# Kernel optimization log

Measured on AMD Instinct MI355X. Metric: run time of the kernel, lower is better.

Reference implementation:

```python
import jax, jax.numpy as jnp
import numpy as np
from jax import lax

B, T, D_IN = 512, 256, 64
N_NEURONS, D_STATE, D_OUT = 2048, 64, 10


def setup_inputs() -> dict:
    key = jax.random.key(0)
    k_seq, k_enc, k_bias, k_gain, k_sd, k_d = jax.random.split(key, 6)
    enc = jax.random.normal(k_enc, (N_NEURONS, D_IN + D_STATE), dtype=jnp.float32)
    # hypersphere strategy: unit-norm encoder rows
    enc = enc / jnp.linalg.norm(enc, axis=-1, keepdims=True)
    return {
        "seq": jax.random.normal(k_seq, (B, T, D_IN), dtype=jnp.float32),
        "encoders": enc,
        "bias": jax.random.normal(k_bias, (N_NEURONS,), dtype=jnp.float32),
        "gain": jax.random.uniform(k_gain, (N_NEURONS,), dtype=jnp.float32),
        "state_decoders": jax.random.normal(k_sd, (N_NEURONS, D_STATE), dtype=jnp.float32) * 0.02,
        "decoders": jax.random.normal(k_d, (N_NEURONS, D_OUT), dtype=jnp.float32) * 0.02,
    }


def reference(seq, encoders, bias, gain, state_decoders, decoders):
    # seq: (B, T, d_in). Recurrent decode-then-re-encode loop over T.
    b = seq.shape[0]
    d_state = state_decoders.shape[1]
    n = encoders.shape[0]

    def step(carry, u_t):
        s, _ = carry  # s: (B, d_state)
        x_aug = jnp.concatenate([u_t, s], axis=-1)  # (B, d_in + d_state)
        a = jnp.abs(gain * (x_aug @ encoders.T) + bias)  # (B, n_neurons), activation='abs'
        s_new = a @ state_decoders  # (B, d_state)
        return (s_new, a), None

    s0 = jnp.zeros((b, d_state), dtype=seq.dtype)
    a0 = jnp.zeros((b, n), dtype=seq.dtype)
    (_, a_final), _ = lax.scan(step, (s0, a0), jnp.swapaxes(seq, 0, 1))
    return a_final @ decoders  # (B, d_out)
```

## Files before the change

### kernel.cpp

```cpp
#include <hip/hip_runtime.h>
#include <math.h>

#define B_    512
#define T_    256
#define DIN   64
#define DS    64
#define KK    128
#define NN    2048
#define DOUT  10

#define NT      512
#define BT      8
#define NTILES  (NN / NT)
#define BTILES  (B_ / BT)
#define THREADS 512
#define NWG     (NTILES * BTILES)

#define PSQ_ELEMS  ((size_t)BTILES * NTILES * BT * DS)
#define PS_FLOATS  (4 * PSQ_ELEMS)
#define ETSW_OFF   PS_FLOATS
#define ETSW_F16   ((size_t)KK * NN)
#define SDSW_OFF   (ETSW_OFF + ETSW_F16 / 2)
#define SDSW_F16   ((size_t)NN * DS)

typedef _Float16 half8 __attribute__((ext_vector_type(8)));
typedef float    f32x4 __attribute__((ext_vector_type(4)));

__global__ __launch_bounds__(256) void pre_kernel(const float* __restrict__ enc,
                                                  const float* __restrict__ sd,
                                                  float* __restrict__ ws,
                                                  float* __restrict__ out) {
    size_t i = (size_t)blockIdx.x * blockDim.x + threadIdx.x;
    size_t stride = (size_t)gridDim.x * blockDim.x;
    unsigned long long* psq = (unsigned long long*)ws;
    for (size_t x = i; x < 2 * PSQ_ELEMS; x += stride) psq[x] = 0ull;
    _Float16* EtSw = (_Float16*)(ws + ETSW_OFF);
    for (size_t x = i; x < (size_t)KK * NN; x += stride) {
        const int j     = (int)(x & 7);
        const int lane  = (int)((x >> 3) & 63);
        const int ktile = (int)((x >> 9) & 3);
        const int ntile = (int)((x >> 11) & 3);
        const int w     = (int)((x >> 13) & 7);
        const int nt    = (int)(x >> 16);
        const int n = nt * 512 + w * 64 + ntile * 16 + (lane & 15);
        const int k = ktile * 32 + ((lane >> 4) << 3) + j;
        EtSw[x] = (_Float16)enc[(size_t)n * KK + k];
    }
    _Float16* SdSw = (_Float16*)(ws + SDSW_OFF);
    for (size_t x = i; x < (size_t)NN * DS; x += stride) {
        const int j     = (int)(x & 7);
        const int lane  = (int)((x >> 3) & 63);
        const int ktile = (int)((x >> 9) & 15);
        const int cg    = (int)((x >> 13) & 3);
        const int nt    = (int)(x >> 15);
        const int n = nt * 512 + ktile * 32 + ((lane >> 4) << 3) + j;
        const int c = cg * 16 + (lane & 15);
        SdSw[x] = (_Float16)sd[(size_t)n * DS + c];
    }
    for (size_t x = i; x < (size_t)B_ * DOUT; x += stride) out[x] = 0.0f;
}

__global__ __launch_bounds__(THREADS, 1) void persist_kernel(
    const float* __restrict__ seq,
    const _Float16* __restrict__ EtSw,
    const _Float16* __restrict__ SdSw,
    const float* __restrict__ bias,
    const float* __restrict__ gain,
    const float* __restrict__ dec,
    unsigned long long* __restrict__ psq,
    float* __restrict__ out)
{
    __shared__ _Float16 xh[16][136];
    __shared__ _Float16 Ash[16][520];

    const int tid = threadIdx.x;
    const int nt = blockIdx.x & (NTILES - 1);
    const int bt = blockIdx.x >> 2;
    const int n0 = nt * NT;
    const int b0 = bt * BT;

    const int w = tid >> 6;
    const int l = tid & 63;
    const int rs = tid >> 6;
    const int cs = tid & 63;
    const int m16 = l & 15;
    const int q8  = (l >> 4) << 3;

    const _Float16* EtW = EtSw + ((size_t)(nt * 8 + w) << 13);
    const _Float16* SdW = SdSw + ((size_t)(nt * 4 + (w & 3)) << 13);

    half8 etf[4][4];
    #pragma unroll
    for (int n4 = 0; n4 < 4; ++n4)
        #pragma unroll
        for (int kt = 0; kt < 4; ++kt)
            etf[n4][kt] = *(const half8*)&EtW[(n4 << 11) + (kt << 9) + (size_t)l * 8];
    half8 sdf[16];
    #pragma unroll
    for (int kt = 0; kt < 16; ++kt)
        sdf[kt] = *(const half8*)&SdW[(kt << 9) + (size_t)l * 8];

    float gv[4], bv[4];
    #pragma unroll
    for (int n4 = 0; n4 < 4; ++n4) {
        gv[n4] = gain[n0 + w * 64 + n4 * 16 + m16];
        bv[n4] = bias[n0 + w * 64 + n4 * 16 + m16];
    }

    const size_t fan_base = ((size_t)bt * NTILES) * BT * DS + (size_t)rs * DS + cs;

    {
        unsigned int* xz = (unsigned int*)&xh[0][0];
        for (int i2 = tid; i2 < 16 * 136 / 2; i2 += THREADS) xz[i2] = 0u;
    }
    __syncthreads();
    if (tid < 128) {
        const int r = tid >> 4, c = (tid & 15) << 2;
        const float4 uv = *(const float4*)&seq[((size_t)(b0 + r) * T_ + 0) * DIN + c];
        _Float16* p = &xh[r][c];
        p[0] = (_Float16)uv.x; p[1] = (_Float16)uv.y;
        p[2] = (_Float16)uv.z; p[3] = (_Float16)uv.w;
    }
    __syncthreads();

    for (int t = 0; t < T_; ++t) {
        const unsigned long long* pb =
            psq + (size_t)((t - 1) & 1) * PSQ_ELEMS + fan_base;
        unsigned long long v0 = 0, v1 = 0, v2 = 0, v3 = 0;
        if (t > 0) {
            v0 = __hip_atomic_load(pb + 0 * (BT * DS), __ATOMIC_RELAXED, __HIP_MEMORY_SCOPE_AGENT);
            v1 = __hip_atomic_load(pb + 1 * (BT * DS), __ATOMIC_RELAXED, __HIP_MEMORY_SCOPE_AGENT);
            v2 = __hip_atomic_load(pb + 2 * (BT * DS), __ATOMIC_RELAXED, __HIP_MEMORY_SCOPE_AGENT);
            v3 = __hip_atomic_load(pb + 3 * (BT * DS), __ATOMIC_RELAXED, __HIP_MEMORY_SCOPE_AGENT);
        }

        f32x4 acc[4];
        #pragma unroll
        for (int n4 = 0; n4 < 4; ++n4) acc[n4] = (f32x4){0.f, 0.f, 0.f, 0.f};
        {
            const half8 af0 = *(const half8*)&xh[m16][q8];
            const half8 af1 = *(const half8*)&xh[m16][32 + q8];
            #pragma unroll
            for (int n4 = 0; n4 < 4; ++n4) {
                acc[n4] = __builtin_amdgcn_mfma_f32_16x16x32_f16(af0, etf[n4][0], acc[n4], 0, 0, 0);
                acc[n4] = __builtin_amdgcn_mfma_f32_16x16x32_f16(af1, etf[n4][1], acc[n4], 0, 0, 0);
            }
        }

        if (t > 0) {
            const unsigned utag = (unsigned)t;
            for (;;) {
                if ((unsigned)(v0 >> 32) == utag && (unsigned)(v1 >> 32) == utag &&
                    (unsigned)(v2 >> 32) == utag && (unsigned)(v3 >> 32) == utag)
                    break;
                v0 = __hip_atomic_load(pb + 0 * (BT * DS), __ATOMIC_RELAXED, __HIP_MEMORY_SCOPE_AGENT);
                v1 = __hip_atomic_load(pb + 1 * (BT * DS), __ATOMIC_RELAXED, __HIP_MEMORY_SCOPE_AGENT);
                v2 = __hip_atomic_load(pb + 2 * (BT * DS), __ATOMIC_RELAXED, __HIP_MEMORY_SCOPE_AGENT);
                v3 = __hip_atomic_load(pb + 3 * (BT * DS), __ATOMIC_RELAXED, __HIP_MEMORY_SCOPE_AGENT);
            }
            const float ssum = __uint_as_float((unsigned)v0) + __uint_as_float((unsigned)v1)
                             + __uint_as_float((unsigned)v2) + __uint_as_float((unsigned)v3);
            xh[rs][DIN + cs] = (_Float16)ssum;
        } else {
            xh[rs][DIN + cs] = (_Float16)0.f;
        }
        __syncthreads();

        {
            const half8 af2 = *(const half8*)&xh[m16][64 + q8];
            const half8 af3 = *(const half8*)&xh[m16][96 + q8];
            #pragma unroll
            for (int n4 = 0; n4 < 4; ++n4) {
                acc[n4] = __builtin_amdgcn_mfma_f32_16x16x32_f16(af2, etf[n4][2], acc[n4], 0, 0, 0);
                acc[n4] = __builtin_amdgcn_mfma_f32_16x16x32_f16(af3, etf[n4][3], acc[n4], 0, 0, 0);
            }
        }

        if (l < 32) {
            const int rq = (l >> 4) << 2;
            #pragma unroll
            for (int n4 = 0; n4 < 4; ++n4) {
                const int n = w * 64 + n4 * 16 + m16;
                Ash[rq + 0][n] = (_Float16)fabsf(gv[n4] * acc[n4][0] + bv[n4]);
                Ash[rq + 1][n] = (_Float16)fabsf(gv[n4] * acc[n4][1] + bv[n4]);
                Ash[rq + 2][n] = (_Float16)fabsf(gv[n4] * acc[n4][2] + bv[n4]);
                Ash[rq + 3][n] = (_Float16)fabsf(gv[n4] * acc[n4][3] + bv[n4]);
            }
        }
        __syncthreads();

        if (t == T_ - 1) {
            for (int idx = tid; idx < BT * DOUT; idx += THREADS) {
                const int r = idx / DOUT;
                const int d = idx % DOUT;
                float o = 0.f;
                #pragma unroll 8
                for (int n = 0; n < NT; ++n)
                    o += (float)Ash[r][n] * dec[(size_t)(n0 + n) * DOUT + d];
                atomicAdd(&out[(size_t)(b0 + r) * DOUT + d], o);
            }
            return;
        }

        if (w < 4) {
            f32x4 d0 = (f32x4){0.f, 0.f, 0.f, 0.f};
            f32x4 d1 = (f32x4){0.f, 0.f, 0.f, 0.f};
            #pragma unroll
            for (int kt = 0; kt < 16; kt += 2) {
                const half8 a0 = *(const half8*)&Ash[m16][kt * 32 + q8];
                d0 = __builtin_amdgcn_mfma_f32_16x16x32_f16(a0, sdf[kt], d0, 0, 0, 0);
                const half8 a1 = *(const half8*)&Ash[m16][(kt + 1) * 32 + q8];
                d1 = __builtin_amdgcn_mfma_f32_16x16x32_f16(a1, sdf[kt + 1], d1, 0, 0, 0);
            }
            d0[0] += d1[0]; d0[1] += d1[1]; d0[2] += d1[2]; d0[3] += d1[3];
            if (l < 32) {
                const int rq = (l >> 4) << 2;
                unsigned long long* pw = psq + (size_t)(t & 1) * PSQ_ELEMS
                    + (((size_t)bt * NTILES + nt) * BT) * DS + 16 * w + m16;
                const unsigned long long tg = (unsigned long long)(unsigned)(t + 1) << 32;
                #pragma unroll
                for (int r = 0; r < 4; ++r) {
                    const float v = d0[rq >= 4 ? r : r] + 0.f;
                    const float vv = d0[r];
                    (void)v;
                    __hip_atomic_store(pw + (size_t)(rq + r) * DS,
                                       tg | (unsigned long long)__float_as_uint(vv),
                                       __ATOMIC_RELAXED, __HIP_MEMORY_SCOPE_AGENT);
                }
            }
        } else if (l < 32) {
            const int idx = ((w - 4) << 5) + l;
            const int r = idx >> 4, c = (idx & 15) << 2;
            const float4 uv =
                *(const float4*)&seq[((size_t)(b0 + r) * T_ + (t + 1)) * DIN + c];
            _Float16* p = &xh[r][c];
            p[0] = (_Float16)uv.x; p[1] = (_Float16)uv.y;
            p[2] = (_Float16)uv.z; p[3] = (_Float16)uv.w;
        }
        __syncthreads();
    }
}

extern "C" void kernel_launch(void* const* d_in, const int* in_sizes, int n_in,
                              void* d_out, int out_size, void* d_ws, size_t ws_size,
                              hipStream_t stream) {
    const float* seq  = (const float*)d_in[0];
    const float* enc  = (const float*)d_in[1];
    const float* bias = (const float*)d_in[2];
    const float* gain = (const float*)d_in[3];
    const float* sd   = (const float*)d_in[4];
    const float* dec  = (const float*)d_in[5];
    float* out = (float*)d_out;
    float* ws  = (float*)d_ws;

    pre_kernel<<<dim3(1024), dim3(256), 0, stream>>>(enc, sd, ws, out);

    unsigned long long* psq = (unsigned long long*)ws;
    const _Float16* EtSw = (const _Float16*)(ws + ETSW_OFF);
    const _Float16* SdSw = (const _Float16*)(ws + SDSW_OFF);

    persist_kernel<<<dim3(NWG), dim3(THREADS), 0, stream>>>(
        seq, EtSw, SdSw, bias, gain, dec, psq, out);
}
```

Baseline: 609.0 us.

## Interleave two independent batch chunks per workgroup to hide cross-workgroup sync latency

Each persistent workgroup now owns two 8-row batch chunks and alternates between them within each timestep. While waiting on the state fan-in flags of one chunk, it computes the other chunk, and it prefetches the other chunk's partial-state loads early. This halves the grid, so each workgroup does twice the serial work, in exchange for overlapping the inter-workgroup spin-wait latency with useful MFMA work. It also doubles LDS use and adds barriers per step.

```diff
diff --git a/kernel.cpp b/kernel.cpp
--- a/kernel.cpp
+++ b/kernel.cpp
@@ -12,11 +12,12 @@
 #define NT      512
 #define BT      8
 #define NTILES  (NN / NT)
-#define BTILES  (B_ / BT)
+#define BTE     (B_ / BT)
+#define BTILES  (BTE / 2)
 #define THREADS 512
 #define NWG     (NTILES * BTILES)
 
-#define PSQ_ELEMS  ((size_t)BTILES * NTILES * BT * DS)
+#define PSQ_ELEMS  ((size_t)BTE * NTILES * BT * DS)
 #define PS_FLOATS  (4 * PSQ_ELEMS)
 #define ETSW_OFF   PS_FLOATS
 #define ETSW_F16   ((size_t)KK * NN)
@@ -70,14 +71,19 @@
     unsigned long long* __restrict__ psq,
     float* __restrict__ out)
 {
-    __shared__ _Float16 xh[16][136];
-    __shared__ _Float16 Ash[16][520];
+    __shared__ _Float16 xhA[16][136];
+    __shared__ _Float16 xhB[16][136];
+    __shared__ _Float16 AshA[16][520];
+    __shared__ _Float16 AshB[16][520];
 
     const int tid = threadIdx.x;
     const int nt = blockIdx.x & (NTILES - 1);
     const int bt = blockIdx.x >> 2;
     const int n0 = nt * NT;
-    const int b0 = bt * BT;
+    const int beA = bt * 2;
+    const int beB = bt * 2 + 1;
+    const int b0A = bt * 16;
+    const int b0B = bt * 16 + 8;
 
     const int w = tid >> 6;
     const int l = tid & 63;
@@ -107,87 +113,95 @@
         bv[n4] = bias[n0 + w * 64 + n4 * 16 + m16];
     }
 
-    const size_t fan_base = ((size_t)bt * NTILES) * BT * DS + (size_t)rs * DS + cs;
+    const size_t fanA = ((size_t)beA * NTILES) * BT * DS + (size_t)rs * DS + cs;
+    const size_t fanB = ((size_t)beB * NTILES) * BT * DS + (size_t)rs * DS + cs;
 
     {
-        unsigned int* xz = (unsigned int*)&xh[0][0];
+        unsigned int* xz = (unsigned int*)&xhA[0][0];
         for (int i2 = tid; i2 < 16 * 136 / 2; i2 += THREADS) xz[i2] = 0u;
+        unsigned int* xz2 = (unsigned int*)&xhB[0][0];
+        for (int i2 = tid; i2 < 16 * 136 / 2; i2 += THREADS) xz2[i2] = 0u;
     }
     __syncthreads();
-    if (tid < 128) {
-        const int r = tid >> 4, c = (tid & 15) << 2;
-        const float4 uv = *(const float4*)&seq[((size_t)(b0 + r) * T_ + 0) * DIN + c];
-        _Float16* p = &xh[r][c];
+    if (tid < 256) {
+        const int ch  = tid >> 7;
+        const int idx = tid & 127;
+        const int r = idx >> 4, c = (idx & 15) << 2;
+        const float4 uv =
+            *(const float4*)&seq[((size_t)((ch ? b0B : b0A) + r) * T_ + 0) * DIN + c];
+        _Float16* p = ch ? &xhB[r][c] : &xhA[r][c];
         p[0] = (_Float16)uv.x; p[1] = (_Float16)uv.y;
         p[2] = (_Float16)uv.z; p[3] = (_Float16)uv.w;
     }
     __syncthreads();
 
+    unsigned long long vA0 = 0, vA1 = 0, vA2 = 0, vA3 = 0;
+    unsigned long long vB0 = 0, vB1 = 0, vB2 = 0, vB3 = 0;
+
     for (int t = 0; t < T_; ++t) {
-        const unsigned long long* pb =
-            psq + (size_t)((t - 1) & 1) * PSQ_ELEMS + fan_base;
-        unsigned long long v0 = 0, v1 = 0, v2 = 0, v3 = 0;
-        if (t > 0) {
-            v0 = __hip_atomic_load(pb + 0 * (BT * DS), __ATOMIC_RELAXED, __HIP_MEMORY_SCOPE_AGENT);
-            v1 = __hip_atomic_load(pb + 1 * (BT * DS), __ATOMIC_RELAXED, __HIP_MEMORY_SCOPE_AGENT);
-            v2 = __hip_atomic_load(pb + 2 * (BT * DS), __ATOMIC_RELAXED, __HIP_MEMORY_SCOPE_AGENT);
-            v3 = __hip_atomic_load(pb + 3 * (BT * DS), __ATOMIC_RELAXED, __HIP_MEMORY_SCOPE_AGENT);
-        }
-
         f32x4 acc[4];
         #pragma unroll
         for (int n4 = 0; n4 < 4; ++n4) acc[n4] = (f32x4){0.f, 0.f, 0.f, 0.f};
         {
-            const half8 af0 = *(const half8*)&xh[m16][q8];
-            const half8 af1 = *(const half8*)&xh[m16][32 + q8];
+            const half8 af0 = *(const half8*)&xhA[m16][q8];
+            const half8 af1 = *(const half8*)&xhA[m16][32 + q8];
             #pragma unroll
             for (int n4 = 0; n4 < 4; ++n4) {
                 acc[n4] = __builtin_amdgcn_mfma_f32_16x16x32_f16(af0, etf[n4][0], acc[n4], 0, 0, 0);
                 acc[n4] = __builtin_amdgcn_mfma_f32_16x16x32_f16(af1, etf[n4][1], acc[n4], 0, 0, 0);
             }
         }
-
         if (t > 0) {
+            const unsigned long long* pbA =
+                psq + (size_t)((t - 1) & 1) * PSQ_ELEMS + fanA;
             const unsigned utag = (unsigned)t;
             for (;;) {
-                if ((unsigned)(v0 >> 32) == utag && (unsigned)(v1 >> 32) == utag &&
-                    (unsigned)(v2 >> 32) == utag && (unsigned)(v3 >> 32) == utag)
+                if ((unsigned)(vA0 >> 32) == utag && (unsigned)(vA1 >> 32) == utag &&
+                    (unsigned)(vA2 >> 32) == utag && (unsigned)(vA3 >> 32) == utag)
                     break;
-                v0 = __hip_atomic_load(pb + 0 * (BT * DS), __ATOMIC_RELAXED, __HIP_MEMORY_SCOPE_AGENT);
-                v1 = __hip_atomic_load(pb + 1 * (BT * DS), __ATOMIC_RELAXED, __HIP_MEMORY_SCOPE_AGENT);
-                v2 = __hip_atomic_load(pb + 2 * (BT * DS), __ATOMIC_RELAXED, __HIP_MEMORY_SCOPE_AGENT);
-                v3 = __hip_atomic_load(pb + 3 * (BT * DS), __ATOMIC_RELAXED, __HIP_MEMORY_SCOPE_AGENT);
-            }
-            const float ssum = __uint_as_float((unsigned)v0) + __uint_as_float((unsigned)v1)
-                             + __uint_as_float((unsigned)v2) + __uint_as_float((unsigned)v3);
-            xh[rs][DIN + cs] = (_Float16)ssum;
+                vA0 = __hip_atomic_load(pbA + 0 * (BT * DS), __ATOMIC_RELAXED, __HIP_MEMORY_SCOPE_AGENT);
+                vA1 = __hip_atomic_load(pbA + 1 * (BT * DS), __ATOMIC_RELAXED, __HIP_MEMORY_SCOPE_AGENT);
+                vA2 = __hip_atomic_load(pbA + 2 * (BT * DS), __ATOMIC_RELAXED, __HIP_MEMORY_SCOPE_AGENT);
+                vA3 = __hip_atomic_load(pbA + 3 * (BT * DS), __ATOMIC_RELAXED, __HIP_MEMORY_SCOPE_AGENT);
+            }
+            const float ssum = __uint_as_float((unsigned)vA0) + __uint_as_float((unsigned)vA1)
+                             + __uint_as_float((unsigned)vA2) + __uint_as_float((unsigned)vA3);
+            xhA[rs][DIN + cs] = (_Float16)ssum;
         } else {
-            xh[rs][DIN + cs] = (_Float16)0.f;
+            xhA[rs][DIN + cs] = (_Float16)0.f;
         }
         __syncthreads();
 
         {
-            const half8 af2 = *(const half8*)&xh[m16][64 + q8];
-            const half8 af3 = *(const half8*)&xh[m16][96 + q8];
+            const half8 af2 = *(const half8*)&xhA[m16][64 + q8];
+            const half8 af3 = *(const half8*)&xhA[m16][96 + q8];
             #pragma unroll
             for (int n4 = 0; n4 < 4; ++n4) {
                 acc[n4] = __builtin_amdgcn_mfma_f32_16x16x32_f16(af2, etf[n4][2], acc[n4], 0, 0, 0);
                 acc[n4] = __builtin_amdgcn_mfma_f32_16x16x32_f16(af3, etf[n4][3], acc[n4], 0, 0, 0);
             }
         }
-
         if (l < 32) {
             const int rq = (l >> 4) << 2;
             #pragma unroll
             for (int n4 = 0; n4 < 4; ++n4) {
                 const int n = w * 64 + n4 * 16 + m16;
-                Ash[rq + 0][n] = (_Float16)fabsf(gv[n4] * acc[n4][0] + bv[n4]);
-                Ash[rq + 1][n] = (_Float16)fabsf(gv[n4] * acc[n4][1] + bv[n4]);
-                Ash[rq + 2][n] = (_Float16)fabsf(gv[n4] * acc[n4][2] + bv[n4]);
-                Ash[rq + 3][n] = (_Float16)fabsf(gv[n4] * acc[n4][3] + bv[n4]);
-            }
-        }
-        __syncthreads();
+                AshA[rq + 0][n] = (_Float16)fabsf(gv[n4] * acc[n4][0] + bv[n4]);
+                AshA[rq + 1][n] = (_Float16)fabsf(gv[n4] * acc[n4][1] + bv[n4]);
+                AshA[rq + 2][n] = (_Float16)fabsf(gv[n4] * acc[n4][2] + bv[n4]);
+                AshA[rq + 3][n] = (_Float16)fabsf(gv[n4] * acc[n4][3] + bv[n4]);
+            }
+        }
+        __syncthreads();
+
+        if (t > 0) {
+            const unsigned long long* pbB =
+                psq + (size_t)((t - 1) & 1) * PSQ_ELEMS + fanB;
+            vB0 = __hip_atomic_load(pbB + 0 * (BT * DS), __ATOMIC_RELAXED, __HIP_MEMORY_SCOPE_AGENT);
+            vB1 = __hip_atomic_load(pbB + 1 * (BT * DS), __ATOMIC_RELAXED, __HIP_MEMORY_SCOPE_AGENT);
+            vB2 = __hip_atomic_load(pbB + 2 * (BT * DS), __ATOMIC_RELAXED, __HIP_MEMORY_SCOPE_AGENT);
+            vB3 = __hip_atomic_load(pbB + 3 * (BT * DS), __ATOMIC_RELAXED, __HIP_MEMORY_SCOPE_AGENT);
+        }
 
         if (t == T_ - 1) {
             for (int idx = tid; idx < BT * DOUT; idx += THREADS) {
@@ -196,46 +210,149 @@
                 float o = 0.f;
                 #pragma unroll 8
                 for (int n = 0; n < NT; ++n)
-                    o += (float)Ash[r][n] * dec[(size_t)(n0 + n) * DOUT + d];
-                atomicAdd(&out[(size_t)(b0 + r) * DOUT + d], o);
-            }
-            return;
-        }
-
-        if (w < 4) {
-            f32x4 d0 = (f32x4){0.f, 0.f, 0.f, 0.f};
-            f32x4 d1 = (f32x4){0.f, 0.f, 0.f, 0.f};
-            #pragma unroll
-            for (int kt = 0; kt < 16; kt += 2) {
-                const half8 a0 = *(const half8*)&Ash[m16][kt * 32 + q8];
-                d0 = __builtin_amdgcn_mfma_f32_16x16x32_f16(a0, sdf[kt], d0, 0, 0, 0);
-                const half8 a1 = *(const half8*)&Ash[m16][(kt + 1) * 32 + q8];
-                d1 = __builtin_amdgcn_mfma_f32_16x16x32_f16(a1, sdf[kt + 1], d1, 0, 0, 0);
-            }
-            d0[0] += d1[0]; d0[1] += d1[1]; d0[2] += d1[2]; d0[3] += d1[3];
-            if (l < 32) {
-                const int rq = (l >> 4) << 2;
-                unsigned long long* pw = psq + (size_t)(t & 1) * PSQ_ELEMS
-                    + (((size_t)bt * NTILES + nt) * BT) * DS + 16 * w + m16;
-                const unsigned long long tg = (unsigned long long)(unsigned)(t + 1) << 32;
+                    o += (float)AshA[r][n] * dec[(size_t)(n0 + n) * DOUT + d];
+                atomicAdd(&out[(size_t)(b0A + r) * DOUT + d], o);
+            }
+        } else {
+            if (w < 4) {
+                f32x4 d0 = (f32x4){0.f, 0.f, 0.f, 0.f};
+                f32x4 d1 = (f32x4){0.f, 0.f, 0.f, 0.f};
                 #pragma unroll
-                for (int r = 0; r < 4; ++r) {
-                    const float v = d0[rq >= 4 ? r : r] + 0.f;
-                    const float vv = d0[r];
-                    (void)v;
-                    __hip_atomic_store(pw + (size_t)(rq + r) * DS,
-                                       tg | (unsigned long long)__float_as_uint(vv),
-                                       __ATOMIC_RELAXED, __HIP_MEMORY_SCOPE_AGENT);
+                for (int kt = 0; kt < 16; kt += 2) {
+                    const half8 a0 = *(const half8*)&AshA[m16][kt * 32 + q8];
+                    d0 = __builtin_amdgcn_mfma_f32_16x16x32_f16(a0, sdf[kt], d0, 0, 0, 0);
+                    const half8 a1 = *(const half8*)&AshA[m16][(kt + 1) * 32 + q8];
+                    d1 = __builtin_amdgcn_mfma_f32_16x16x32_f16(a1, sdf[kt + 1], d1, 0, 0, 0);
                 }
-            }
-        } else if (l < 32) {
-            const int idx = ((w - 4) << 5) + l;
-            const int r = idx >> 4, c = (idx & 15) << 2;
-            const float4 uv =
-                *(const float4*)&seq[((size_t)(b0 + r) * T_ + (t + 1)) * DIN + c];
-            _Float16* p = &xh[r][c];
-            p[0] = (_Float16)uv.x; p[1] = (_Float16)uv.y;
-            p[2] = (_Float16)uv.z; p[3] = (_Float16)uv.w;
+                d0[0] += d1[0]; d0[1] += d1[1]; d0[2] += d1[2]; d0[3] += d1[3];
+                if (l < 32) {
+                    const int rq = (l >> 4) << 2;
+                    unsigned long long* pw = psq + (size_t)(t & 1) * PSQ_ELEMS
+                        + (((size_t)beA * NTILES + nt) * BT) * DS + 16 * w + m16;
+                    const unsigned long long tg = (unsigned long long)(unsigned)(t + 1) << 32;
+                    #pragma unroll
+                    for (int r = 0; r < 4; ++r) {
+                        __hip_atomic_store(pw + (size_t)(rq + r) * DS,
+                                           tg | (unsigned long long)__float_as_uint(d0[r]),
+                                           __ATOMIC_RELAXED, __HIP_MEMORY_SCOPE_AGENT);
+                    }
+                }
+            } else if (l < 32) {
+                const int idx = ((w - 4) << 5) + l;
+                const int r = idx >> 4, c = (idx & 15) << 2;
+                const float4 uv =
+                    *(const float4*)&seq[((size_t)(b0A + r) * T_ + (t + 1)) * DIN + c];
+                _Float16* p = &xhA[r][c];
+                p[0] = (_Float16)uv.x; p[1] = (_Float16)uv.y;
+                p[2] = (_Float16)uv.z; p[3] = (_Float16)uv.w;
+            }
+        }
+        __syncthreads();
+
+        #pragma unroll
+        for (int n4 = 0; n4 < 4; ++n4) acc[n4] = (f32x4){0.f, 0.f, 0.f, 0.f};
+        {
+            const half8 af0 = *(const half8*)&xhB[m16][q8];
+            const half8 af1 = *(const half8*)&xhB[m16][32 + q8];
+            #pragma unroll
+            for (int n4 = 0; n4 < 4; ++n4) {
+                acc[n4] = __builtin_amdgcn_mfma_f32_16x16x32_f16(af0, etf[n4][0], acc[n4], 0, 0, 0);
+                acc[n4] = __builtin_amdgcn_mfma_f32_16x16x32_f16(af1, etf[n4][1], acc[n4], 0, 0, 0);
+            }
+        }
+        if (t > 0) {
+            const unsigned long long* pbB =
+                psq + (size_t)((t - 1) & 1) * PSQ_ELEMS + fanB;
+            const unsigned utag = (unsigned)t;
+            for (;;) {
+                if ((unsigned)(vB0 >> 32) == utag && (unsigned)(vB1 >> 32) == utag &&
+                    (unsigned)(vB2 >> 32) == utag && (unsigned)(vB3 >> 32) == utag)
+                    break;
+                vB0 = __hip_atomic_load(pbB + 0 * (BT * DS), __ATOMIC_RELAXED, __HIP_MEMORY_SCOPE_AGENT);
+                vB1 = __hip_atomic_load(pbB + 1 * (BT * DS), __ATOMIC_RELAXED, __HIP_MEMORY_SCOPE_AGENT);
+                vB2 = __hip_atomic_load(pbB + 2 * (BT * DS), __ATOMIC_RELAXED, __HIP_MEMORY_SCOPE_AGENT);
+                vB3 = __hip_atomic_load(pbB + 3 * (BT * DS), __ATOMIC_RELAXED, __HIP_MEMORY_SCOPE_AGENT);
+            }
+            const float ssum = __uint_as_float((unsigned)vB0) + __uint_as_float((unsigned)vB1)
+                             + __uint_as_float((unsigned)vB2) + __uint_as_float((unsigned)vB3);
+            xhB[rs][DIN + cs] = (_Float16)ssum;
+        } else {
+            xhB[rs][DIN + cs] = (_Float16)0.f;
+        }
+        __syncthreads();
+
+        {
+            const half8 af2 = *(const half8*)&xhB[m16][64 + q8];
+            const half8 af3 = *(const half8*)&xhB[m16][96 + q8];
+            #pragma unroll
+            for (int n4 = 0; n4 < 4; ++n4) {
+                acc[n4] = __builtin_amdgcn_mfma_f32_16x16x32_f16(af2, etf[n4][2], acc[n4], 0, 0, 0);
+                acc[n4] = __builtin_amdgcn_mfma_f32_16x16x32_f16(af3, etf[n4][3], acc[n4], 0, 0, 0);
+            }
+        }
+        if (l < 32) {
+            const int rq = (l >> 4) << 2;
+            #pragma unroll
+            for (int n4 = 0; n4 < 4; ++n4) {
+                const int n = w * 64 + n4 * 16 + m16;
+                AshB[rq + 0][n] = (_Float16)fabsf(gv[n4] * acc[n4][0] + bv[n4]);
+                AshB[rq + 1][n] = (_Float16)fabsf(gv[n4] * acc[n4][1] + bv[n4]);
+                AshB[rq + 2][n] = (_Float16)fabsf(gv[n4] * acc[n4][2] + bv[n4]);
+                AshB[rq + 3][n] = (_Float16)fabsf(gv[n4] * acc[n4][3] + bv[n4]);
+            }
+        }
+        __syncthreads();
+
+        if (t == T_ - 1) {
+            for (int idx = tid; idx < BT * DOUT; idx += THREADS) {
+                const int r = idx / DOUT;
+                const int d = idx % DOUT;
+                float o = 0.f;
+                #pragma unroll 8
+                for (int n = 0; n < NT; ++n)
+                    o += (float)AshB[r][n] * dec[(size_t)(n0 + n) * DOUT + d];
+                atomicAdd(&out[(size_t)(b0B + r) * DOUT + d], o);
+            }
+        } else {
+            const unsigned long long* pbA =
+                psq + (size_t)(t & 1) * PSQ_ELEMS + fanA;
+            vA0 = __hip_atomic_load(pbA + 0 * (BT * DS), __ATOMIC_RELAXED, __HIP_MEMORY_SCOPE_AGENT);
+            vA1 = __hip_atomic_load(pbA + 1 * (BT * DS), __ATOMIC_RELAXED, __HIP_MEMORY_SCOPE_AGENT);
+            vA2 = __hip_atomic_load(pbA + 2 * (BT * DS), __ATOMIC_RELAXED, __HIP_MEMORY_SCOPE_AGENT);
+            vA3 = __hip_atomic_load(pbA + 3 * (BT * DS), __ATOMIC_RELAXED, __HIP_MEMORY_SCOPE_AGENT);
+
+            if (w < 4) {
+                f32x4 d0 = (f32x4){0.f, 0.f, 0.f, 0.f};
+                f32x4 d1 = (f32x4){0.f, 0.f, 0.f, 0.f};
+                #pragma unroll
+                for (int kt = 0; kt < 16; kt += 2) {
+                    const half8 a0 = *(const half8*)&AshB[m16][kt * 32 + q8];
+                    d0 = __builtin_amdgcn_mfma_f32_16x16x32_f16(a0, sdf[kt], d0, 0, 0, 0);
+                    const half8 a1 = *(const half8*)&AshB[m16][(kt + 1) * 32 + q8];
+                    d1 = __builtin_amdgcn_mfma_f32_16x16x32_f16(a1, sdf[kt + 1], d1, 0, 0, 0);
+                }
+                d0[0] += d1[0]; d0[1] += d1[1]; d0[2] += d1[2]; d0[3] += d1[3];
+                if (l < 32) {
+                    const int rq = (l >> 4) << 2;
+                    unsigned long long* pw = psq + (size_t)(t & 1) * PSQ_ELEMS
+                        + (((size_t)beB * NTILES + nt) * BT) * DS + 16 * w + m16;
+                    const unsigned long long tg = (unsigned long long)(unsigned)(t + 1) << 32;
+                    #pragma unroll
+                    for (int r = 0; r < 4; ++r) {
+                        __hip_atomic_store(pw + (size_t)(rq + r) * DS,
+                                           tg | (unsigned long long)__float_as_uint(d0[r]),
+                                           __ATOMIC_RELAXED, __HIP_MEMORY_SCOPE_AGENT);
+                    }
+                }
+            } else if (l < 32) {
+                const int idx = ((w - 4) << 5) + l;
+                const int r = idx >> 4, c = (idx & 15) << 2;
+                const float4 uv =
+                    *(const float4*)&seq[((size_t)(b0B + r) * T_ + (t + 1)) * DIN + c];
+                _Float16* p = &xhB[r][c];
+                p[0] = (_Float16)uv.x; p[1] = (_Float16)uv.y;
+                p[2] = (_Float16)uv.z; p[3] = (_Float16)uv.w;
+            }
         }
         __syncthreads();
     }
```

Measured after the change: 916.2 us. +50.4%, slower.

## Add sc0 fast-path exchange buffer with agent-scope fallback and XCD-aware block mapping

Applied to the files above, without the earlier changes.

Adds a second partial-state buffer. Producers store each value twice: once with sc0-only stores, meant to stay coherent within the shared L2 of one XCD, and once with agent-scope atomics. Consumers poll the fast buffer with sc0 loads for a few tries, then fall back to polling the agent-scope buffer. Blocks are remapped so the four n-tiles that exchange data for a batch tile land on the same XCD (blockIdx mod 8). The goal is to cut the latency of the cross-workgroup handoff each timestep, at the cost of doubled stores and reliance on the round-robin XCD dispatch assumption.

```diff
diff --git a/kernel.cpp b/kernel.cpp
--- a/kernel.cpp
+++ b/kernel.cpp
@@ -17,14 +17,30 @@
 #define NWG     (NTILES * BTILES)
 
 #define PSQ_ELEMS  ((size_t)BTILES * NTILES * BT * DS)
-#define PS_FLOATS  (4 * PSQ_ELEMS)
-#define ETSW_OFF   PS_FLOATS
+#define SLOW_OFF_F (4 * PSQ_ELEMS)
+#define ETSW_OFF   (8 * PSQ_ELEMS)
 #define ETSW_F16   ((size_t)KK * NN)
 #define SDSW_OFF   (ETSW_OFF + ETSW_F16 / 2)
 #define SDSW_F16   ((size_t)NN * DS)
 
 typedef _Float16 half8 __attribute__((ext_vector_type(8)));
 typedef float    f32x4 __attribute__((ext_vector_type(4)));
+
+__device__ __forceinline__ void ld4_sc0(const unsigned long long* p0,
+                                        const unsigned long long* p1,
+                                        const unsigned long long* p2,
+                                        const unsigned long long* p3,
+                                        unsigned long long& v0, unsigned long long& v1,
+                                        unsigned long long& v2, unsigned long long& v3) {
+    asm volatile("global_load_dwordx2 %0, %4, off sc0\n\t"
+                 "global_load_dwordx2 %1, %5, off sc0\n\t"
+                 "global_load_dwordx2 %2, %6, off sc0\n\t"
+                 "global_load_dwordx2 %3, %7, off sc0\n\t"
+                 "s_waitcnt vmcnt(0)"
+                 : "=&v"(v0), "=&v"(v1), "=&v"(v2), "=&v"(v3)
+                 : "v"(p0), "v"(p1), "v"(p2), "v"(p3)
+                 : "memory");
+}
 
 __global__ __launch_bounds__(256) void pre_kernel(const float* __restrict__ enc,
                                                   const float* __restrict__ sd,
@@ -33,7 +49,7 @@
     size_t i = (size_t)blockIdx.x * blockDim.x + threadIdx.x;
     size_t stride = (size_t)gridDim.x * blockDim.x;
     unsigned long long* psq = (unsigned long long*)ws;
-    for (size_t x = i; x < 2 * PSQ_ELEMS; x += stride) psq[x] = 0ull;
+    for (size_t x = i; x < 4 * PSQ_ELEMS; x += stride) psq[x] = 0ull;
     _Float16* EtSw = (_Float16*)(ws + ETSW_OFF);
     for (size_t x = i; x < (size_t)KK * NN; x += stride) {
         const int j     = (int)(x & 7);
@@ -67,15 +83,18 @@
     const float* __restrict__ bias,
     const float* __restrict__ gain,
     const float* __restrict__ dec,
-    unsigned long long* __restrict__ psq,
+    unsigned long long* __restrict__ psqF,
+    unsigned long long* __restrict__ psqS,
     float* __restrict__ out)
 {
     __shared__ _Float16 xh[16][136];
     __shared__ _Float16 Ash[16][520];
 
     const int tid = threadIdx.x;
-    const int nt = blockIdx.x & (NTILES - 1);
-    const int bt = blockIdx.x >> 2;
+    const int r8 = blockIdx.x & 7;
+    const int s  = blockIdx.x >> 3;
+    const int nt = s & 3;
+    const int bt = r8 * 8 + (s >> 2);
     const int n0 = nt * NT;
     const int b0 = bt * BT;
 
@@ -124,14 +143,20 @@
     __syncthreads();
 
     for (int t = 0; t < T_; ++t) {
-        const unsigned long long* pb =
-            psq + (size_t)((t - 1) & 1) * PSQ_ELEMS + fan_base;
+        const unsigned long long* pbF =
+            psqF + (size_t)((t - 1) & 1) * PSQ_ELEMS + fan_base;
+        const unsigned long long* pbS =
+            psqS + (size_t)((t - 1) & 1) * PSQ_ELEMS + fan_base;
         unsigned long long v0 = 0, v1 = 0, v2 = 0, v3 = 0;
         if (t > 0) {
-            v0 = __hip_atomic_load(pb + 0 * (BT * DS), __ATOMIC_RELAXED, __HIP_MEMORY_SCOPE_AGENT);
-            v1 = __hip_atomic_load(pb + 1 * (BT * DS), __ATOMIC_RELAXED, __HIP_MEMORY_SCOPE_AGENT);
-            v2 = __hip_atomic_load(pb + 2 * (BT * DS), __ATOMIC_RELAXED, __HIP_MEMORY_SCOPE_AGENT);
-            v3 = __hip_atomic_load(pb + 3 * (BT * DS), __ATOMIC_RELAXED, __HIP_MEMORY_SCOPE_AGENT);
+            asm volatile("global_load_dwordx2 %0, %4, off sc0\n\t"
+                         "global_load_dwordx2 %1, %5, off sc0\n\t"
+                         "global_load_dwordx2 %2, %6, off sc0\n\t"
+                         "global_load_dwordx2 %3, %7, off sc0"
+                         : "=&v"(v0), "=&v"(v1), "=&v"(v2), "=&v"(v3)
+                         : "v"(pbF + 0 * (BT * DS)), "v"(pbF + 1 * (BT * DS)),
+                           "v"(pbF + 2 * (BT * DS)), "v"(pbF + 3 * (BT * DS))
+                         : "memory");
         }
 
         f32x4 acc[4];
@@ -148,15 +173,28 @@
         }
 
         if (t > 0) {
+            asm volatile("s_waitcnt vmcnt(0)" ::: "memory");
+            __builtin_amdgcn_sched_barrier(0);
             const unsigned utag = (unsigned)t;
+            int tries = 0;
+            bool ok;
             for (;;) {
-                if ((unsigned)(v0 >> 32) == utag && (unsigned)(v1 >> 32) == utag &&
-                    (unsigned)(v2 >> 32) == utag && (unsigned)(v3 >> 32) == utag)
-                    break;
-                v0 = __hip_atomic_load(pb + 0 * (BT * DS), __ATOMIC_RELAXED, __HIP_MEMORY_SCOPE_AGENT);
-                v1 = __hip_atomic_load(pb + 1 * (BT * DS), __ATOMIC_RELAXED, __HIP_MEMORY_SCOPE_AGENT);
-                v2 = __hip_atomic_load(pb + 2 * (BT * DS), __ATOMIC_RELAXED, __HIP_MEMORY_SCOPE_AGENT);
-                v3 = __hip_atomic_load(pb + 3 * (BT * DS), __ATOMIC_RELAXED, __HIP_MEMORY_SCOPE_AGENT);
+                ok = ((unsigned)(v0 >> 32) == utag && (unsigned)(v1 >> 32) == utag &&
+                      (unsigned)(v2 >> 32) == utag && (unsigned)(v3 >> 32) == utag);
+                if (ok || ++tries > 8) break;
+                ld4_sc0(pbF + 0 * (BT * DS), pbF + 1 * (BT * DS),
+                        pbF + 2 * (BT * DS), pbF + 3 * (BT * DS), v0, v1, v2, v3);
+            }
+            if (!ok) {
+                for (;;) {
+                    v0 = __hip_atomic_load(pbS + 0 * (BT * DS), __ATOMIC_RELAXED, __HIP_MEMORY_SCOPE_AGENT);
+                    v1 = __hip_atomic_load(pbS + 1 * (BT * DS), __ATOMIC_RELAXED, __HIP_MEMORY_SCOPE_AGENT);
+                    v2 = __hip_atomic_load(pbS + 2 * (BT * DS), __ATOMIC_RELAXED, __HIP_MEMORY_SCOPE_AGENT);
+                    v3 = __hip_atomic_load(pbS + 3 * (BT * DS), __ATOMIC_RELAXED, __HIP_MEMORY_SCOPE_AGENT);
+                    if ((unsigned)(v0 >> 32) == utag && (unsigned)(v1 >> 32) == utag &&
+                        (unsigned)(v2 >> 32) == utag && (unsigned)(v3 >> 32) == utag)
+                        break;
+                }
             }
             const float ssum = __uint_as_float((unsigned)v0) + __uint_as_float((unsigned)v1)
                              + __uint_as_float((unsigned)v2) + __uint_as_float((unsigned)v3);
@@ -215,16 +253,19 @@
             d0[0] += d1[0]; d0[1] += d1[1]; d0[2] += d1[2]; d0[3] += d1[3];
             if (l < 32) {
                 const int rq = (l >> 4) << 2;
-                unsigned long long* pw = psq + (size_t)(t & 1) * PSQ_ELEMS
+                const size_t slot = (size_t)(t & 1) * PSQ_ELEMS
                     + (((size_t)bt * NTILES + nt) * BT) * DS + 16 * w + m16;
+                unsigned long long* pwF = psqF + slot;
+                unsigned long long* pwS = psqS + slot;
                 const unsigned long long tg = (unsigned long long)(unsigned)(t + 1) << 32;
                 #pragma unroll
                 for (int r = 0; r < 4; ++r) {
-                    const float v = d0[rq >= 4 ? r : r] + 0.f;
-                    const float vv = d0[r];
-                    (void)v;
-                    __hip_atomic_store(pw + (size_t)(rq + r) * DS,
-                                       tg | (unsigned long long)__float_as_uint(vv),
+                    const unsigned long long val =
+                        tg | (unsigned long long)__float_as_uint(d0[r]);
+                    asm volatile("global_store_dwordx2 %0, %1, off sc0"
+                                 :: "v"(pwF + (size_t)(rq + r) * DS), "v"(val)
+                                 : "memory");
+                    __hip_atomic_store(pwS + (size_t)(rq + r) * DS, val,
                                        __ATOMIC_RELAXED, __HIP_MEMORY_SCOPE_AGENT);
                 }
             }
@@ -255,10 +296,11 @@
 
     pre_kernel<<<dim3(1024), dim3(256), 0, stream>>>(enc, sd, ws, out);
 
-    unsigned long long* psq = (unsigned long long*)ws;
+    unsigned long long* psqF = (unsigned long long*)ws;
+    unsigned long long* psqS = (unsigned long long*)(ws + SLOW_OFF_F);
     const _Float16* EtSw = (const _Float16*)(ws + ETSW_OFF);
     const _Float16* SdSw = (const _Float16*)(ws + SDSW_OFF);
 
     persist_kernel<<<dim3(NWG), dim3(THREADS), 0, stream>>>(
-        seq, EtSw, SdSw, bias, gain, dec, psq, out);
+        seq, EtSw, SdSw, bias, gain, dec, psqF, psqS, out);
 }
```

New measurement: 869.1 us. +42.7%, slower.
